# Kernel tuning notes

Hardware: AMD Instinct MI355X
Metric: run time of the kernel (lower is better)

Reference implementation:

```python
import jax, jax.numpy as jnp
import numpy as np
from jax import lax

B, T = 4, 1024
V, C, H, L = 50257, 768, 12, 12
D = C // H           # head size = 64
FF = 4 * C           # ffn hidden = 3072
EPS = 1e-5


def setup_inputs() -> dict:
    key = jax.random.key(0)
    ks = jax.random.split(key, 20)
    s = 0.02
    inp = {
        'x': jax.random.randint(ks[0], (B, T), 0, V, dtype=jnp.int32),
        'y': jax.random.randint(ks[1], (B, T), 0, V, dtype=jnp.int32),
        'tok_emb': jax.random.normal(ks[2], (V, C), jnp.float32) * s,
        'pos_emb': jax.random.normal(ks[3], (V, C), jnp.float32) * s,
        'Wk': jax.random.normal(ks[4], (L, H, C, D), jnp.float32) * s,
        'Wq': jax.random.normal(ks[5], (L, H, C, D), jnp.float32) * s,
        'Wv': jax.random.normal(ks[6], (L, H, C, D), jnp.float32) * s,
        'Wproj': jax.random.normal(ks[7], (L, C, C), jnp.float32) * s,
        'bproj': jnp.zeros((L, C), jnp.float32),
        'ln1_g': jnp.ones((L, C), jnp.float32),
        'ln1_b': jnp.zeros((L, C), jnp.float32),
        'W1': jax.random.normal(ks[8], (L, C, FF), jnp.float32) * s,
        'b1': jnp.zeros((L, FF), jnp.float32),
        'W2': jax.random.normal(ks[9], (L, FF, C), jnp.float32) * s,
        'b2': jnp.zeros((L, C), jnp.float32),
        'ln2_g': jnp.ones((L, C), jnp.float32),
        'ln2_b': jnp.zeros((L, C), jnp.float32),
        'Wlm': jax.random.normal(ks[10], (C, V), jnp.float32) * s,
        'blm': jnp.zeros((V,), jnp.float32),
    }
    return inp


def _layernorm(x, g, b):
    m = jnp.mean(x, axis=-1, keepdims=True)
    v = jnp.var(x, axis=-1, keepdims=True)
    return (x - m) * lax.rsqrt(v + EPS) * g + b


def _forward(x, tok_emb, pos_emb, Wk, Wq, Wv, Wproj, bproj, ln1_g, ln1_b,
             W1, b1, W2, b2, ln2_g, ln2_b, Wlm, blm):
    # NOTE: the original indexes the position embedding table with token ids x.
    h = tok_emb[x] + pos_emb[x]                      # [B,T,C]
    mask = jnp.tril(jnp.ones((T, T), bool))          # causal tril buffer
    scale = D ** -0.5

    def layer(h, p):
        wk, wq, wv, wp, bp, g1, be1, w1, bb1, w2, bb2, g2, be2 = p
        k = jnp.einsum('btc,hcd->bhtd', h, wk)
        q = jnp.einsum('btc,hcd->bhtd', h, wq)
        v = jnp.einsum('btc,hcd->bhtd', h, wv)
        # faithful quirk: k @ q^T (rows=k index, cols=q index)
        wei = jnp.einsum('bhtd,bhsd->bhts', k, q) * scale
        wei = jnp.where(mask, wei, -jnp.inf)
        wei = jax.nn.softmax(wei, axis=-1)
        o = jnp.einsum('bhts,bhsd->bhtd', wei, v)    # [B,H,T,D]
        o = o.transpose(0, 2, 1, 3).reshape(B, T, C) # concat heads
        attn = o @ wp + bp
        h = _layernorm(h + attn, g1, be1)
        ff = jax.nn.relu(h @ w1 + bb1) @ w2 + bb2
        h = _layernorm(h + ff, g2, be2)
        return h, None

    params = (Wk, Wq, Wv, Wproj, bproj, ln1_g, ln1_b, W1, b1, W2, b2, ln2_g, ln2_b)
    h, _ = lax.scan(layer, h, params)
    logits = h @ Wlm + blm                           # [B,T,V]
    return logits


def reference(x, y, tok_emb, pos_emb, Wk, Wq, Wv, Wproj, bproj, ln1_g, ln1_b,
              W1, b1, W2, b2, ln2_g, ln2_b, Wlm, blm):
    logits = _forward(x, tok_emb, pos_emb, Wk, Wq, Wv, Wproj, bproj,
                      ln1_g, ln1_b, W1, b1, W2, b2, ln2_g, ln2_b, Wlm, blm)
    logp = jax.nn.log_softmax(logits, axis=-1)
    loss = -jnp.mean(jnp.take_along_axis(logp, y[..., None].astype(jnp.int32), axis=-1))
    return logits, loss
```

## Files before the change

### kernel.cpp

```cpp
#include <hip/hip_runtime.h>
#include <hip/hip_bf16.h>
#include <math.h>

#define BB 4
#define TT 1024
#define VV 50257
#define VPAD2 50432
#define CC 768
#define HH 12
#define DD 64
#define LL 12
#define FFH 3072
#define MROWS (BB*TT)
#define QBLK 128
#define KVBLK 64
#define NPART (VPAD2 / 64)

typedef __bf16 bf16x8 __attribute__((ext_vector_type(8)));
typedef float  f32x4  __attribute__((ext_vector_type(4)));
typedef unsigned int u32;
#define AS1 __attribute__((address_space(1)))
#define AS3 __attribute__((address_space(3)))

static __device__ __forceinline__ void gload_lds16(const void* g, void* l) {
    __builtin_amdgcn_global_load_lds((const AS1 u32*)g, (AS3 u32*)l, 16, 0, 0);
}

static __device__ __forceinline__ void stage_tile(const __hip_bfloat16* __restrict__ A,
                                                  const __hip_bfloat16* __restrict__ Bt,
                                                  int Kld, int k0, int bm, int bn,
                                                  int w, int l, char* As, char* Bs) {
    #pragma unroll
    for (int it = 0; it < 4; it++) {
        int chunk = w * 4 + it;
        int o = chunk * 1024 + l * 16;
        int row = o >> 7;
        int cb = (o & 127) ^ ((row & 7) << 4);
        gload_lds16(A + (size_t)(bm + row) * Kld + k0 + (cb >> 1), As + chunk * 1024);
        gload_lds16(Bt + (size_t)(bn + row) * Kld + k0 + (cb >> 1), Bs + chunk * 1024);
    }
}

static __device__ __forceinline__ void stage_tile256_k32(const __hip_bfloat16* __restrict__ A,
                                                         const __hip_bfloat16* __restrict__ Bt,
                                                         int Kld, int k0, int bm, int bn,
                                                         int w, int l, char* As, char* Bs) {
    #pragma unroll
    for (int it = 0; it < 2; it++) {
        int chunk = w * 2 + it;
        int o = chunk * 1024 + l * 16;
        int row = o >> 6;
        int cb = (o & 63) ^ ((row & 3) << 4);
        gload_lds16(A + (size_t)(bm + row) * Kld + k0 + (cb >> 1), As + chunk * 1024);
        gload_lds16(Bt + (size_t)(bn + row) * Kld + k0 + (cb >> 1), Bs + chunk * 1024);
    }
}

__global__ void embed_kernel(const int* __restrict__ x, const float* __restrict__ tok,
                             const float* __restrict__ pos, float* __restrict__ h,
                             __hip_bfloat16* __restrict__ hb) {
    int idx = blockIdx.x * 256 + threadIdx.x;
    if (idx >= MROWS * CC) return;
    int row = idx / CC, c = idx - row * CC;
    int id = x[row];
    float v = tok[(size_t)id * CC + c] + pos[(size_t)id * CC + c];
    h[idx] = v;
    hb[idx] = __float2bfloat16(v);
}

__global__ __launch_bounds__(256) void cvtT_mat(const float* __restrict__ in,
                                                __hip_bfloat16* __restrict__ out,
                                                int K, int Nin,
                                                size_t ibs, size_t obs) {
    __shared__ float t[32][33];
    const float* ip = in + blockIdx.z * ibs;
    __hip_bfloat16* op = out + blockIdx.z * obs;
    int n0 = blockIdx.x * 32, k0 = blockIdx.y * 32;
    int tx = threadIdx.x & 31, ty = threadIdx.x >> 5;
    #pragma unroll
    for (int i = 0; i < 4; i++) {
        int k = k0 + ty + i * 8, n = n0 + tx;
        t[ty + i * 8][tx] = (n < Nin) ? ip[(size_t)k * Nin + n] : 0.f;
    }
    __syncthreads();
    #pragma unroll
    for (int i = 0; i < 4; i++) {
        int n = n0 + ty + i * 8, k = k0 + tx;
        op[(size_t)n * K + k] = __float2bfloat16(t[tx][ty + i * 8]);
    }
}

__global__ __launch_bounds__(256) void cvtT_qkv(const float* __restrict__ Wk,
                                                const float* __restrict__ Wq,
                                                const float* __restrict__ Wv,
                                                __hip_bfloat16* __restrict__ kT,
                                                __hip_bfloat16* __restrict__ qT,
                                                __hip_bfloat16* __restrict__ vT) {
    int z = blockIdx.z;
    int tensor = z / 144, lh = z % 144;
    int l = lh / HH, hh = lh % HH;
    const float* in = (tensor == 0 ? Wk : tensor == 1 ? Wq : Wv) + (size_t)lh * CC * DD;
    __hip_bfloat16* out = (tensor == 0 ? kT : tensor == 1 ? qT : vT)
                          + ((size_t)l * CC + hh * DD) * CC;
    __shared__ float t[32][33];
    int c0 = blockIdx.x * 32, d0 = blockIdx.y * 32;
    int tx = threadIdx.x & 31, ty = threadIdx.x >> 5;
    #pragma unroll
    for (int i = 0; i < 4; i++)
        t[ty + i * 8][tx] = in[(size_t)(c0 + ty + i * 8) * DD + d0 + tx];
    __syncthreads();
    #pragma unroll
    for (int i = 0; i < 4; i++)
        out[(size_t)(d0 + ty + i * 8) * CC + c0 + tx] = __float2bfloat16(t[tx][ty + i * 8]);
}

__global__ __launch_bounds__(256) void gemm_mfma(const __hip_bfloat16* __restrict__ A,
                                                 const __hip_bfloat16* __restrict__ Bt,
                                                 const float* __restrict__ bias,
                                                 float* __restrict__ Cf,
                                                 __hip_bfloat16* __restrict__ Cb,
                                                 int M, int N, int K, int relu) {
    __shared__ __align__(16) char smem[65536];
    int tid = threadIdx.x;
    int l = tid & 63, w = tid >> 6;
    int wr = w >> 1, wc = w & 1;
    int bm = blockIdx.y * 128, bn = blockIdx.x * 128;

    f32x4 acc[4][4] = {};

    stage_tile(A, Bt, K, 0, bm, bn, w, l, smem, smem + 32768);
    int p = 0;
    for (int k0 = 0; k0 < K; k0 += 64) {
        __syncthreads();
        if (k0 + 64 < K)
            stage_tile(A, Bt, K, k0 + 64, bm, bn, w, l,
                       smem + (p ^ 1) * 16384, smem + 32768 + (p ^ 1) * 16384);
        const char* Ab = smem + p * 16384;
        const char* Bb = smem + 32768 + p * 16384;
        #pragma unroll
        for (int ks = 0; ks < 2; ks++) {
            bf16x8 af[4], bfr[4];
            #pragma unroll
            for (int i = 0; i < 4; i++) {
                int row = wr * 64 + i * 16 + (l & 15);
                int cb = (ks * 64 + (l >> 4) * 16) ^ ((row & 7) << 4);
                af[i] = *(const bf16x8*)(Ab + row * 128 + cb);
            }
            #pragma unroll
            for (int j = 0; j < 4; j++) {
                int row = wc * 64 + j * 16 + (l & 15);
                int cb = (ks * 64 + (l >> 4) * 16) ^ ((row & 7) << 4);
                bfr[j] = *(const bf16x8*)(Bb + row * 128 + cb);
            }
            #pragma unroll
            for (int i = 0; i < 4; i++)
                #pragma unroll
                for (int j = 0; j < 4; j++)
                    acc[i][j] = __builtin_amdgcn_mfma_f32_16x16x32_bf16(af[i], bfr[j], acc[i][j], 0, 0, 0);
        }
        p ^= 1;
    }

    if (Cb) {
        __hip_bfloat16* ebh = (__hip_bfloat16*)smem;
        __syncthreads();
        #pragma unroll
        for (int i = 0; i < 4; i++) {
            #pragma unroll
            for (int j = 0; j < 4; j++) {
                int colt = wc * 64 + j * 16 + (l & 15);
                float bv = bias ? bias[bn + colt] : 0.f;
                #pragma unroll
                for (int r = 0; r < 4; r++) {
                    int rowc = wr * 64 + i * 16 + (l >> 4) * 4 + r;
                    float v = acc[i][j][r] + bv;
                    if (relu) v = fmaxf(v, 0.f);
                    ebh[rowc * 136 + colt] = __float2bfloat16(v);
                }
            }
        }
        __syncthreads();
        #pragma unroll
        for (int pass = 0; pass < 8; pass++) {
            int idx = pass * 256 + tid;
            int rowc = idx >> 4, colq = idx & 15;
            *(bf16x8*)&Cb[(size_t)(bm + rowc) * N + bn + colq * 8] =
                *(const bf16x8*)&ebh[rowc * 136 + colq * 8];
        }
    } else {
        float* eb = (float*)smem;
        #pragma unroll
        for (int c = 0; c < 2; c++) {
            __syncthreads();
            if (wr == c) {
                #pragma unroll
                for (int i = 0; i < 4; i++) {
                    #pragma unroll
                    for (int j = 0; j < 4; j++) {
                        int colt = wc * 64 + j * 16 + (l & 15);
                        float bv = bias ? bias[bn + colt] : 0.f;
                        #pragma unroll
                        for (int r = 0; r < 4; r++) {
                            int rowc = i * 16 + (l >> 4) * 4 + r;
                            float v = acc[i][j][r] + bv;
                            if (relu) v = fmaxf(v, 0.f);
                            eb[rowc * 132 + colt] = v;
                        }
                    }
                }
            }
            __syncthreads();
            #pragma unroll
            for (int pass = 0; pass < 8; pass++) {
                int idx = pass * 256 + tid;
                int rowc = idx >> 5, colq = idx & 31;
                *(f32x4*)&Cf[(size_t)(bm + c * 64 + rowc) * N + bn + colq * 4] =
                    *(const f32x4*)&eb[rowc * 132 + colq * 4];
            }
        }
    }
}

__global__ __launch_bounds__(512) void lm_head_mfma256(const __hip_bfloat16* __restrict__ A,
                                                       const __hip_bfloat16* __restrict__ Bt,
                                                       const float* __restrict__ bias,
                                                       float* __restrict__ Cf,
                                                       float* __restrict__ pm,
                                                       float* __restrict__ ps) {
    __shared__ __align__(16) char smem[65536];
    int tid = threadIdx.x;
    int l = tid & 63, w = tid >> 6;
    int wr = w >> 2, wc = w & 3;
    int bm = blockIdx.x * 256, bn = blockIdx.y * 256;

    f32x4 acc[8][4] = {};

    stage_tile256_k32(A, Bt, CC, 0, bm, bn, w, l, smem, smem + 32768);
    int p = 0;
    for (int k0 = 0; k0 < CC; k0 += 32) {
        __syncthreads();
        if (k0 + 32 < CC)
            stage_tile256_k32(A, Bt, CC, k0 + 32, bm, bn, w, l,
                              smem + (p ^ 1) * 16384, smem + 32768 + (p ^ 1) * 16384);
        const char* Ab = smem + p * 16384;
        const char* Bb = smem + 32768 + p * 16384;
        bf16x8 af[8], bfr[4];
        #pragma unroll
        for (int i = 0; i < 8; i++) {
            int row = wr * 128 + i * 16 + (l & 15);
            int cb = ((l >> 4) * 16) ^ ((row & 3) << 4);
            af[i] = *(const bf16x8*)(Ab + row * 64 + cb);
        }
        #pragma unroll
        for (int j = 0; j < 4; j++) {
            int row = wc * 64 + j * 16 + (l & 15);
            int cb = ((l >> 4) * 16) ^ ((row & 3) << 4);
            bfr[j] = *(const bf16x8*)(Bb + row * 64 + cb);
        }
        #pragma unroll
        for (int i = 0; i < 8; i++)
            #pragma unroll
            for (int j = 0; j < 4; j++)
                acc[i][j] = __builtin_amdgcn_mfma_f32_16x16x32_bf16(af[i], bfr[j], acc[i][j], 0, 0, 0);
        p ^= 1;
    }

    #pragma unroll
    for (int j = 0; j < 4; j++) {
        int col = bn + wc * 64 + j * 16 + (l & 15);
        float bv = (col < VV) ? bias[col] : 0.f;
        #pragma unroll
        for (int i = 0; i < 8; i++)
            #pragma unroll
            for (int r = 0; r < 4; r++)
                acc[i][j][r] += bv;
    }

    int pidx = blockIdx.y * 4 + wc;
    #pragma unroll
    for (int i = 0; i < 8; i++) {
        int row = bm + wr * 128 + i * 16 + (l >> 4) * 4;
        #pragma unroll
        for (int r = 0; r < 4; r++) {
            float pv[4];
            float rmax = -1e30f;
            #pragma unroll
            for (int j = 0; j < 4; j++) {
                int col = bn + wc * 64 + j * 16 + (l & 15);
                float v = (col < VV) ? acc[i][j][r] : -1e30f;
                pv[j] = v;
                rmax = fmaxf(rmax, v);
            }
            #pragma unroll
            for (int msk = 1; msk < 16; msk <<= 1)
                rmax = fmaxf(rmax, __shfl_xor(rmax, msk));
            float s = 0.f;
            #pragma unroll
            for (int j = 0; j < 4; j++) s += __expf(pv[j] - rmax);
            #pragma unroll
            for (int msk = 1; msk < 16; msk <<= 1)
                s += __shfl_xor(s, msk);
            if ((l & 15) == 0) {
                pm[(size_t)(row + r) * NPART + pidx] = rmax;
                ps[(size_t)(row + r) * NPART + pidx] = s;
            }
        }
    }

    float* eb = (float*)smem;
    #pragma unroll
    for (int c = 0; c < 8; c++) {
        __syncthreads();
        if (wr == (c >> 2)) {
            int i0 = (c & 3) * 2;
            #pragma unroll
            for (int ii = 0; ii < 2; ii++) {
                #pragma unroll
                for (int j = 0; j < 4; j++) {
                    int colt = wc * 64 + j * 16 + (l & 15);
                    #pragma unroll
                    for (int r = 0; r < 4; r++) {
                        int rowc = ii * 16 + (l >> 4) * 4 + r;
                        eb[rowc * 264 + colt] = acc[i0 + ii][j][r];
                    }
                }
            }
        }
        __syncthreads();
        #pragma unroll
        for (int pass = 0; pass < 16; pass++) {
            int idx = pass * 512 + tid;
            int rowc = idx >> 8, colq = idx & 255;
            int col = bn + colq;
            if (col < VV)
                Cf[(size_t)(bm + c * 32 + rowc) * VV + col] = eb[rowc * 264 + colq];
        }
    }
}

__global__ __launch_bounds__(256) void nll_combine(const float* __restrict__ pm,
                                                   const float* __restrict__ ps,
                                                   const float* __restrict__ logits,
                                                   const int* __restrict__ y,
                                                   float* __restrict__ rl) {
    int m = blockIdx.x, tid = threadIdx.x;
    __shared__ float rm[256], rs[256];
    float mt = -1e30f, st = 0.f;
    for (int i = tid; i < NPART; i += 256) {
        float mi = pm[(size_t)m * NPART + i];
        float si = ps[(size_t)m * NPART + i];
        float mn = fmaxf(mt, mi);
        st = st * __expf(mt - mn) + si * __expf(mi - mn);
        mt = mn;
    }
    rm[tid] = mt; rs[tid] = st; __syncthreads();
    for (int off = 128; off > 0; off >>= 1) {
        if (tid < off) {
            float ma = rm[tid], mb = rm[tid + off];
            float mn = fmaxf(ma, mb);
            rs[tid] = rs[tid] * __expf(ma - mn) + rs[tid + off] * __expf(mb - mn);
            rm[tid] = mn;
        }
        __syncthreads();
    }
    if (tid == 0)
        rl[m] = logf(rs[0]) + rm[0] - logits[(size_t)m * VV + y[m]];
}

__global__ __launch_bounds__(256) void gemm_qkv_mfma(const __hip_bfloat16* __restrict__ A,
                                                     const __hip_bfloat16* __restrict__ kT,
                                                     const __hip_bfloat16* __restrict__ qT,
                                                     const __hip_bfloat16* __restrict__ vT,
                                                     __hip_bfloat16* __restrict__ ko,
                                                     __hip_bfloat16* __restrict__ qo,
                                                     __hip_bfloat16* __restrict__ vto) {
    const __hip_bfloat16* Bt = (blockIdx.z == 0) ? kT : (blockIdx.z == 1) ? qT : vT;
    __shared__ __align__(16) char smem[65536];
    int tid = threadIdx.x;
    int l = tid & 63, w = tid >> 6;
    int wr = w >> 1, wc = w & 1;
    int bm = blockIdx.y * 128, bn = blockIdx.x * 128;

    f32x4 acc[4][4] = {};

    stage_tile(A, Bt, CC, 0, bm, bn, w, l, smem, smem + 32768);
    int p = 0;
    for (int k0 = 0; k0 < CC; k0 += 64) {
        __syncthreads();
        if (k0 + 64 < CC)
            stage_tile(A, Bt, CC, k0 + 64, bm, bn, w, l,
                       smem + (p ^ 1) * 16384, smem + 32768 + (p ^ 1) * 16384);
        const char* Ab = smem + p * 16384;
        const char* Bb = smem + 32768 + p * 16384;
        #pragma unroll
        for (int ks = 0; ks < 2; ks++) {
            bf16x8 af[4], bfr[4];
            #pragma unroll
            for (int i = 0; i < 4; i++) {
                int row = wr * 64 + i * 16 + (l & 15);
                int cb = (ks * 64 + (l >> 4) * 16) ^ ((row & 7) << 4);
                af[i] = *(const bf16x8*)(Ab + row * 128 + cb);
            }
            #pragma unroll
            for (int j = 0; j < 4; j++) {
                int row = wc * 64 + j * 16 + (l & 15);
                int cb = (ks * 64 + (l >> 4) * 16) ^ ((row & 7) << 4);
                bfr[j] = *(const bf16x8*)(Bb + row * 128 + cb);
            }
            #pragma unroll
            for (int i = 0; i < 4; i++)
                #pragma unroll
                for (int j = 0; j < 4; j++)
                    acc[i][j] = __builtin_amdgcn_mfma_f32_16x16x32_bf16(af[i], bfr[j], acc[i][j], 0, 0, 0);
        }
        p ^= 1;
    }

    int zz = blockIdx.z;
    int b = bm >> 10, tbase = bm & 1023;
    __hip_bfloat16* eb = (__hip_bfloat16*)smem;
    __syncthreads();
    if (zz != 2) {
        #pragma unroll
        for (int i = 0; i < 4; i++)
            #pragma unroll
            for (int j = 0; j < 4; j++) {
                int colt = wc * 64 + j * 16 + (l & 15);
                #pragma unroll
                for (int r = 0; r < 4; r++) {
                    int rowc = wr * 64 + i * 16 + (l >> 4) * 4 + r;
                    eb[rowc * 136 + colt] = __float2bfloat16(acc[i][j][r]);
                }
            }
        __syncthreads();
        __hip_bfloat16* O = (zz == 0) ? ko : qo;
        #pragma unroll
        for (int pass = 0; pass < 8; pass++) {
            int idx = pass * 256 + tid;
            int rowc = idx >> 4, colq = idx & 15;
            int head = (bn >> 6) + (colq >> 3);
            int d = (colq & 7) * 8;
            int t = tbase + rowc;
            *(bf16x8*)&O[(((size_t)(b * HH + head)) * TT + t) * DD + d] =
                *(const bf16x8*)&eb[rowc * 136 + colq * 8];
        }
    } else {
        #pragma unroll
        for (int i = 0; i < 4; i++)
            #pragma unroll
            for (int j = 0; j < 4; j++) {
                int colt = wc * 64 + j * 16 + (l & 15);
                #pragma unroll
                for (int r = 0; r < 4; r++) {
                    int rowc = wr * 64 + i * 16 + (l >> 4) * 4 + r;
                    eb[colt * 136 + rowc] = __float2bfloat16(acc[i][j][r]);
                }
            }
        __syncthreads();
        #pragma unroll
        for (int pass = 0; pass < 8; pass++) {
            int idx = pass * 256 + tid;
            int line = idx >> 4, tq = idx & 15;
            int head = (bn >> 6) + (line >> 6);
            int d = line & 63;
            *(bf16x8*)&vto[(((size_t)(b * HH + head)) * DD + d) * TT + tbase + tq * 8] =
                *(const bf16x8*)&eb[line * 136 + tq * 8];
        }
    }
}

__global__ __launch_bounds__(256) void attn_mfma(const __hip_bfloat16* __restrict__ kq,
                                                 const __hip_bfloat16* __restrict__ qk,
                                                 const __hip_bfloat16* __restrict__ vt,
                                                 __hip_bfloat16* __restrict__ oc) {
    __shared__ __hip_bfloat16 Qs[2][KVBLK * 64];
    __shared__ __hip_bfloat16 Vs[2][64 * KVBLK];
    __shared__ __hip_bfloat16 Ps[QBLK * KVBLK];
    int tid = threadIdx.x;
    int l = tid & 63, w = tid >> 6;
    int t0 = blockIdx.x * QBLK;
    size_t bh = (size_t)(blockIdx.z * HH + blockIdx.y);
    const __hip_bfloat16* kqp = kq + bh * TT * DD;
    const __hip_bfloat16* qkp = qk + bh * TT * DD;
    const __hip_bfloat16* vtp = vt + bh * DD * TT;

    bf16x8 af[2][2];
    #pragma unroll
    for (int i = 0; i < 2; i++)
        #pragma unroll
        for (int ks = 0; ks < 2; ks++)
            af[i][ks] = *(const bf16x8*)&kqp[(size_t)(t0 + w * 32 + i * 16 + (l & 15)) * DD
                                             + ks * 32 + (l >> 4) * 8];

    f32x4 acc_o[2][4] = {};
    float mrow[2][4], lrow[2][4];
    #pragma unroll
    for (int i = 0; i < 2; i++)
        #pragma unroll
        for (int r = 0; r < 4; r++) { mrow[i][r] = -1e30f; lrow[i][r] = 0.f; }

    auto stageKV = [&](int pp, int s0) {
        #pragma unroll
        for (int it = 0; it < 2; it++) {
            int chunk = w * 2 + it;
            int o = chunk * 1024 + l * 16;
            int row = o >> 7;
            int cb = (o & 127) ^ ((row & 7) << 4);
            gload_lds16(qkp + (size_t)(s0 + row) * DD + (cb >> 1),
                        (char*)Qs[pp] + chunk * 1024);
            gload_lds16(vtp + (size_t)row * TT + s0 + (cb >> 1),
                        (char*)Vs[pp] + chunk * 1024);
        }
    };

    int nt = (t0 + QBLK) / KVBLK;
    stageKV(0, 0);
    int p = 0;
    for (int ti = 0; ti < nt; ti++) {
        int s0 = ti * KVBLK;
        __syncthreads();
        if (ti + 1 < nt) stageKV(p ^ 1, s0 + KVBLK);

        f32x4 sa[2][4] = {};
        #pragma unroll
        for (int ks = 0; ks < 2; ks++) {
            bf16x8 bfr[4];
            #pragma unroll
            for (int j = 0; j < 4; j++) {
                int row = j * 16 + (l & 15);
                int cb = (ks * 64 + (l >> 4) * 16) ^ ((row & 7) << 4);
                bfr[j] = *(const bf16x8*)((const char*)Qs[p] + row * 128 + cb);
            }
            #pragma unroll
            for (int i = 0; i < 2; i++)
                #pragma unroll
                for (int j = 0; j < 4; j++)
                    sa[i][j] = __builtin_amdgcn_mfma_f32_16x16x32_bf16(af[i][ks], bfr[j], sa[i][j], 0, 0, 0);
        }

        #pragma unroll
        for (int i = 0; i < 2; i++) {
            #pragma unroll
            for (int r = 0; r < 4; r++) {
                int t = t0 + w * 32 + i * 16 + (l >> 4) * 4 + r;
                float pv[4];
                float rmax = -1e30f;
                #pragma unroll
                for (int j = 0; j < 4; j++) {
                    int s = s0 + j * 16 + (l & 15);
                    float v = sa[i][j][r] * 0.125f;
                    v = (s <= t) ? v : -1e30f;
                    pv[j] = v;
                    rmax = fmaxf(rmax, v);
                }
                #pragma unroll
                for (int msk = 1; msk < 16; msk <<= 1)
                    rmax = fmaxf(rmax, __shfl_xor(rmax, msk));
                float mo = mrow[i][r];
                float mn = fmaxf(mo, rmax);
                float fac = __expf(mo - mn);
                float ls = 0.f;
                int prow = w * 32 + i * 16 + (l >> 4) * 4 + r;
                #pragma unroll
                for (int j = 0; j < 4; j++) {
                    float e = __expf(pv[j] - mn);
                    ls += e;
                    int cb = (j * 32 + (l & 15) * 2) ^ ((prow & 7) << 4);
                    *(__hip_bfloat16*)((char*)Ps + prow * 128 + cb) = __float2bfloat16(e);
                }
                #pragma unroll
                for (int msk = 1; msk < 16; msk <<= 1)
                    ls += __shfl_xor(ls, msk);
                mrow[i][r] = mn;
                lrow[i][r] = lrow[i][r] * fac + ls;
                #pragma unroll
                for (int jd = 0; jd < 4; jd++)
                    acc_o[i][jd][r] *= fac;
            }
        }

        #pragma unroll
        for (int ks = 0; ks < 2; ks++) {
            bf16x8 pa[2], vf[4];
            #pragma unroll
            for (int i = 0; i < 2; i++) {
                int row = w * 32 + i * 16 + (l & 15);
                int cb = (ks * 64 + (l >> 4) * 16) ^ ((row & 7) << 4);
                pa[i] = *(const bf16x8*)((const char*)Ps + row * 128 + cb);
            }
            #pragma unroll
            for (int jd = 0; jd < 4; jd++) {
                int row = jd * 16 + (l & 15);
                int cb = (ks * 64 + (l >> 4) * 16) ^ ((row & 7) << 4);
                vf[jd] = *(const bf16x8*)((const char*)Vs[p] + row * 128 + cb);
            }
            #pragma unroll
            for (int i = 0; i < 2; i++)
                #pragma unroll
                for (int jd = 0; jd < 4; jd++)
                    acc_o[i][jd] = __builtin_amdgcn_mfma_f32_16x16x32_bf16(pa[i], vf[jd], acc_o[i][jd], 0, 0, 0);
        }
        p ^= 1;
    }

    int b = blockIdx.z, hh = blockIdx.y;
    #pragma unroll
    for (int i = 0; i < 2; i++) {
        #pragma unroll
        for (int r = 0; r < 4; r++) {
            float inv = 1.f / lrow[i][r];
            int t = t0 + w * 32 + i * 16 + (l >> 4) * 4 + r;
            #pragma unroll
            for (int jd = 0; jd < 4; jd++) {
                int d = jd * 16 + (l & 15);
                oc[((size_t)(b * TT + t)) * CC + hh * DD + d] =
                    __float2bfloat16(acc_o[i][jd][r] * inv);
            }
        }
    }
}

__global__ __launch_bounds__(256) void resid_ln(float* __restrict__ h,
                                                const float* __restrict__ t,
                                                const float* __restrict__ g,
                                                const float* __restrict__ bta,
                                                __hip_bfloat16* __restrict__ hb) {
    int row = blockIdx.x;
    int tid = threadIdx.x;
    __shared__ float red[256];
    float x[3];
    float s = 0.f;
    #pragma unroll
    for (int i = 0; i < 3; i++) {
        int c = tid + i * 256;
        x[i] = h[(size_t)row * CC + c] + t[(size_t)row * CC + c];
        s += x[i];
    }
    red[tid] = s; __syncthreads();
    for (int off = 128; off > 0; off >>= 1) {
        if (tid < off) red[tid] += red[tid + off];
        __syncthreads();
    }
    float mean = red[0] * (1.f / CC); __syncthreads();
    float s2 = 0.f;
    #pragma unroll
    for (int i = 0; i < 3; i++) { float dd = x[i] - mean; s2 += dd * dd; }
    red[tid] = s2; __syncthreads();
    for (int off = 128; off > 0; off >>= 1) {
        if (tid < off) red[tid] += red[tid + off];
        __syncthreads();
    }
    float inv = rsqrtf(red[0] * (1.f / CC) + 1e-5f);
    #pragma unroll
    for (int i = 0; i < 3; i++) {
        int c = tid + i * 256;
        float o = (x[i] - mean) * inv * g[c] + bta[c];
        h[(size_t)row * CC + c] = o;
        hb[(size_t)row * CC + c] = __float2bfloat16(o);
    }
}

__global__ __launch_bounds__(256) void loss_reduce(const float* __restrict__ rl,
                                                   float* __restrict__ out) {
    int tid = threadIdx.x;
    __shared__ float red[256];
    float s = 0.f;
    for (int i = tid; i < MROWS; i += 256) s += rl[i];
    red[tid] = s; __syncthreads();
    for (int off = 128; off > 0; off >>= 1) {
        if (tid < off) red[tid] += red[tid + off];
        __syncthreads();
    }
    if (tid == 0) out[0] = red[0] * (1.f / MROWS);
}

extern "C" void kernel_launch(void* const* d_in, const int* in_sizes, int n_in,
                              void* d_out, int out_size, void* d_ws, size_t ws_size,
                              hipStream_t stream) {
    const int*   x     = (const int*)d_in[0];
    const int*   y     = (const int*)d_in[1];
    const float* tok   = (const float*)d_in[2];
    const float* pos   = (const float*)d_in[3];
    const float* Wk    = (const float*)d_in[4];
    const float* Wq    = (const float*)d_in[5];
    const float* Wv    = (const float*)d_in[6];
    const float* Wproj = (const float*)d_in[7];
    const float* bproj = (const float*)d_in[8];
    const float* ln1g  = (const float*)d_in[9];
    const float* ln1b  = (const float*)d_in[10];
    const float* W1    = (const float*)d_in[11];
    const float* b1    = (const float*)d_in[12];
    const float* W2    = (const float*)d_in[13];
    const float* b2    = (const float*)d_in[14];
    const float* ln2g  = (const float*)d_in[15];
    const float* ln2b  = (const float*)d_in[16];
    const float* Wlm   = (const float*)d_in[17];
    const float* blm   = (const float*)d_in[18];

    float* logits = (float*)d_out;
    float* lossp  = (float*)d_out + ((size_t)out_size - 1);

    char* p = (char*)d_ws;
    auto alloc = [&](size_t bytes) { char* r = p; p += (bytes + 255) & ~255ULL; return r; };
    const size_t S_HC = (size_t)MROWS * CC;

    float* h    = (float*)alloc(S_HC * 4);
    float* tmpf = (float*)alloc(S_HC * 4);
    float* rl   = (float*)alloc(MROWS * 4);
    float* pm   = (float*)alloc((size_t)MROWS * NPART * 4);
    float* ps   = (float*)alloc((size_t)MROWS * NPART * 4);
    __hip_bfloat16* kbb  = (__hip_bfloat16*)alloc(S_HC * 2);
    __hip_bfloat16* qbb  = (__hip_bfloat16*)alloc(S_HC * 2);
    __hip_bfloat16* vtb  = (__hip_bfloat16*)alloc(S_HC * 2);
    __hip_bfloat16* hb   = (__hip_bfloat16*)alloc(S_HC * 2);
    __hip_bfloat16* ocb  = (__hip_bfloat16*)alloc(S_HC * 2);
    __hip_bfloat16* ff1b = (__hip_bfloat16*)alloc((size_t)MROWS * FFH * 2);
    __hip_bfloat16* kT   = (__hip_bfloat16*)alloc((size_t)LL * CC * CC * 2);
    __hip_bfloat16* qT   = (__hip_bfloat16*)alloc((size_t)LL * CC * CC * 2);
    __hip_bfloat16* vT   = (__hip_bfloat16*)alloc((size_t)LL * CC * CC * 2);
    __hip_bfloat16* pT   = (__hip_bfloat16*)alloc((size_t)LL * CC * CC * 2);
    __hip_bfloat16* w1T  = (__hip_bfloat16*)alloc((size_t)LL * CC * FFH * 2);
    __hip_bfloat16* w2T  = (__hip_bfloat16*)alloc((size_t)LL * FFH * CC * 2);
    __hip_bfloat16* lmT  = (__hip_bfloat16*)alloc((size_t)VPAD2 * CC * 2);

    dim3 blk(256);

    cvtT_qkv<<<dim3(24, 2, 3 * 144), blk, 0, stream>>>(Wk, Wq, Wv, kT, qT, vT);
    cvtT_mat<<<dim3(24, 24, LL), blk, 0, stream>>>(Wproj, pT, CC, CC,
                                                   (size_t)CC * CC, (size_t)CC * CC);
    cvtT_mat<<<dim3(96, 24, LL), blk, 0, stream>>>(W1, w1T, CC, FFH,
                                                   (size_t)CC * FFH, (size_t)FFH * CC);
    cvtT_mat<<<dim3(24, 96, LL), blk, 0, stream>>>(W2, w2T, FFH, CC,
                                                   (size_t)FFH * CC, (size_t)CC * FFH);
    cvtT_mat<<<dim3(VPAD2 / 32, 24, 1), blk, 0, stream>>>(Wlm, lmT, CC, VV, 0, 0);

    embed_kernel<<<dim3((MROWS * CC + 255) / 256), blk, 0, stream>>>(x, tok, pos, h, hb);

    for (int l = 0; l < LL; l++) {
        const __hip_bfloat16* kT_l = kT + (size_t)l * CC * CC;
        const __hip_bfloat16* qT_l = qT + (size_t)l * CC * CC;
        const __hip_bfloat16* vT_l = vT + (size_t)l * CC * CC;
        const __hip_bfloat16* pT_l = pT + (size_t)l * CC * CC;
        const __hip_bfloat16* w1T_l = w1T + (size_t)l * CC * FFH;
        const __hip_bfloat16* w2T_l = w2T + (size_t)l * FFH * CC;

        gemm_qkv_mfma<<<dim3(CC / 128, MROWS / 128, 3), blk, 0, stream>>>(
            hb, kT_l, qT_l, vT_l, kbb, qbb, vtb);
        attn_mfma<<<dim3(TT / QBLK, HH, BB), blk, 0, stream>>>(kbb, qbb, vtb, ocb);
        gemm_mfma<<<dim3(CC / 128, MROWS / 128), blk, 0, stream>>>(
            ocb, pT_l, bproj + (size_t)l * CC, tmpf, (__hip_bfloat16*)nullptr,
            MROWS, CC, CC, 0);
        resid_ln<<<dim3(MROWS), blk, 0, stream>>>(h, tmpf, ln1g + (size_t)l * CC,
                                                  ln1b + (size_t)l * CC, hb);
        gemm_mfma<<<dim3(FFH / 128, MROWS / 128), blk, 0, stream>>>(
            hb, w1T_l, b1 + (size_t)l * FFH, (float*)nullptr, ff1b,
            MROWS, FFH, CC, 1);
        gemm_mfma<<<dim3(CC / 128, MROWS / 128), blk, 0, stream>>>(
            ff1b, w2T_l, b2 + (size_t)l * CC, tmpf, (__hip_bfloat16*)nullptr,
            MROWS, CC, FFH, 0);
        resid_ln<<<dim3(MROWS), blk, 0, stream>>>(h, tmpf, ln2g + (size_t)l * CC,
                                                  ln2b + (size_t)l * CC, hb);
    }

    lm_head_mfma256<<<dim3(MROWS / 256, VPAD2 / 256), dim3(512), 0, stream>>>(
        hb, lmT, blm, logits, pm, ps);
    nll_combine<<<dim3(MROWS), blk, 0, stream>>>(pm, ps, logits, y, rl);
    loss_reduce<<<dim3(1), blk, 0, stream>>>(rl, lossp);
}
```

Before: 3.336 ms.

## Use K=64 tiles in LM head GEMM and per-wave epilogue without block barriers

The LM-head GEMM now stages K=64 slices per double-buffered step, using 128 KB of LDS with an 8-way XOR swizzle, which halves the number of loop iterations and block barriers. The epilogue gives each wave its own LDS scratch, double-buffered, so it can transpose its own 16-row chunks and write logits without block-wide __syncthreads. The cost is higher LDS use, which may limit occupancy. The per-wave epilogue writes rows of 64 columns, which may coalesce less well than the previous 256-wide rows.

```diff
diff --git a/kernel.cpp b/kernel.cpp
--- a/kernel.cpp
+++ b/kernel.cpp
@@ -41,16 +41,16 @@
     }
 }
 
-static __device__ __forceinline__ void stage_tile256_k32(const __hip_bfloat16* __restrict__ A,
-                                                         const __hip_bfloat16* __restrict__ Bt,
-                                                         int Kld, int k0, int bm, int bn,
-                                                         int w, int l, char* As, char* Bs) {
-    #pragma unroll
-    for (int it = 0; it < 2; it++) {
-        int chunk = w * 2 + it;
+static __device__ __forceinline__ void stage_tile256(const __hip_bfloat16* __restrict__ A,
+                                                     const __hip_bfloat16* __restrict__ Bt,
+                                                     int Kld, int k0, int bm, int bn,
+                                                     int w, int l, char* As, char* Bs) {
+    #pragma unroll
+    for (int it = 0; it < 4; it++) {
+        int chunk = w * 4 + it;
         int o = chunk * 1024 + l * 16;
-        int row = o >> 6;
-        int cb = (o & 63) ^ ((row & 3) << 4);
+        int row = o >> 7;
+        int cb = (o & 127) ^ ((row & 7) << 4);
         gload_lds16(A + (size_t)(bm + row) * Kld + k0 + (cb >> 1), As + chunk * 1024);
         gload_lds16(Bt + (size_t)(bn + row) * Kld + k0 + (cb >> 1), Bs + chunk * 1024);
     }
@@ -227,7 +227,7 @@
                                                        float* __restrict__ Cf,
                                                        float* __restrict__ pm,
                                                        float* __restrict__ ps) {
-    __shared__ __align__(16) char smem[65536];
+    __shared__ __align__(16) char smem[131072];
     int tid = threadIdx.x;
     int l = tid & 63, w = tid >> 6;
     int wr = w >> 2, wc = w & 3;
@@ -235,33 +235,36 @@
 
     f32x4 acc[8][4] = {};
 
-    stage_tile256_k32(A, Bt, CC, 0, bm, bn, w, l, smem, smem + 32768);
+    stage_tile256(A, Bt, CC, 0, bm, bn, w, l, smem, smem + 65536);
     int p = 0;
-    for (int k0 = 0; k0 < CC; k0 += 32) {
-        __syncthreads();
-        if (k0 + 32 < CC)
-            stage_tile256_k32(A, Bt, CC, k0 + 32, bm, bn, w, l,
-                              smem + (p ^ 1) * 16384, smem + 32768 + (p ^ 1) * 16384);
-        const char* Ab = smem + p * 16384;
-        const char* Bb = smem + 32768 + p * 16384;
-        bf16x8 af[8], bfr[4];
-        #pragma unroll
-        for (int i = 0; i < 8; i++) {
-            int row = wr * 128 + i * 16 + (l & 15);
-            int cb = ((l >> 4) * 16) ^ ((row & 3) << 4);
-            af[i] = *(const bf16x8*)(Ab + row * 64 + cb);
-        }
-        #pragma unroll
-        for (int j = 0; j < 4; j++) {
-            int row = wc * 64 + j * 16 + (l & 15);
-            int cb = ((l >> 4) * 16) ^ ((row & 3) << 4);
-            bfr[j] = *(const bf16x8*)(Bb + row * 64 + cb);
-        }
-        #pragma unroll
-        for (int i = 0; i < 8; i++)
-            #pragma unroll
-            for (int j = 0; j < 4; j++)
-                acc[i][j] = __builtin_amdgcn_mfma_f32_16x16x32_bf16(af[i], bfr[j], acc[i][j], 0, 0, 0);
+    for (int k0 = 0; k0 < CC; k0 += 64) {
+        __syncthreads();
+        if (k0 + 64 < CC)
+            stage_tile256(A, Bt, CC, k0 + 64, bm, bn, w, l,
+                          smem + (p ^ 1) * 32768, smem + 65536 + (p ^ 1) * 32768);
+        const char* Ab = smem + p * 32768;
+        const char* Bb = smem + 65536 + p * 32768;
+        #pragma unroll
+        for (int ks = 0; ks < 2; ks++) {
+            bf16x8 af[8], bfr[4];
+            #pragma unroll
+            for (int i = 0; i < 8; i++) {
+                int row = wr * 128 + i * 16 + (l & 15);
+                int cb = (ks * 64 + (l >> 4) * 16) ^ ((row & 7) << 4);
+                af[i] = *(const bf16x8*)(Ab + row * 128 + cb);
+            }
+            #pragma unroll
+            for (int j = 0; j < 4; j++) {
+                int row = wc * 64 + j * 16 + (l & 15);
+                int cb = (ks * 64 + (l >> 4) * 16) ^ ((row & 7) << 4);
+                bfr[j] = *(const bf16x8*)(Bb + row * 128 + cb);
+            }
+            #pragma unroll
+            for (int i = 0; i < 8; i++)
+                #pragma unroll
+                for (int j = 0; j < 4; j++)
+                    acc[i][j] = __builtin_amdgcn_mfma_f32_16x16x32_bf16(af[i], bfr[j], acc[i][j], 0, 0, 0);
+        }
         p ^= 1;
     }
 
@@ -307,33 +310,28 @@
         }
     }
 
-    float* eb = (float*)smem;
-    #pragma unroll
-    for (int c = 0; c < 8; c++) {
-        __syncthreads();
-        if (wr == (c >> 2)) {
-            int i0 = (c & 3) * 2;
-            #pragma unroll
-            for (int ii = 0; ii < 2; ii++) {
-                #pragma unroll
-                for (int j = 0; j < 4; j++) {
-                    int colt = wc * 64 + j * 16 + (l & 15);
-                    #pragma unroll
-                    for (int r = 0; r < 4; r++) {
-                        int rowc = ii * 16 + (l >> 4) * 4 + r;
-                        eb[rowc * 264 + colt] = acc[i0 + ii][j][r];
-                    }
-                }
-            }
-        }
-        __syncthreads();
-        #pragma unroll
-        for (int pass = 0; pass < 16; pass++) {
-            int idx = pass * 512 + tid;
-            int rowc = idx >> 8, colq = idx & 255;
-            int col = bn + colq;
-            if (col < VV)
-                Cf[(size_t)(bm + c * 32 + rowc) * VV + col] = eb[rowc * 264 + colq];
+    __syncthreads();
+    float* eb0 = (float*)smem + (size_t)(w * 2 + 0) * (16 * 68);
+    float* eb1 = (float*)smem + (size_t)(w * 2 + 1) * (16 * 68);
+    int colg = bn + wc * 64 + l;
+    bool valid = colg < VV;
+    #pragma unroll
+    for (int i = 0; i < 8; i++) {
+        float* eb = (i & 1) ? eb1 : eb0;
+        #pragma unroll
+        for (int j = 0; j < 4; j++) {
+            int colt = j * 16 + (l & 15);
+            #pragma unroll
+            for (int r = 0; r < 4; r++) {
+                int rowc = (l >> 4) * 4 + r;
+                eb[rowc * 68 + colt] = acc[i][j][r];
+            }
+        }
+        int rowbase = bm + wr * 128 + i * 16;
+        #pragma unroll
+        for (int pp = 0; pp < 16; pp++) {
+            float v = eb[pp * 68 + l];
+            if (valid) Cf[(size_t)(rowbase + pp) * VV + colg] = v;
         }
     }
 }
```

New measurement: 3.288 ms. About the same (-1.5%).
